# Performance work log

Hardware: AMD Instinct MI355X
Metric: run time of the kernel (lower is better)

## Reference

```python
import jax, jax.numpy as jnp
import numpy as np

MODES = 2
LC = 4
N = 6000
KNN = 10
NODES = 64
CH = MODES ** 2
M = N * 2 * (KNN + 1)  # total candidate couplings


def setup_inputs() -> dict:
    key = jax.random.key(0)
    ks = jax.random.split(key, 6)
    return {
        "CK_inputs": jax.random.normal(ks[0], (N, 2 * (KNN + 1), 3), dtype=jnp.float32),
        "W_in": jax.random.normal(ks[1], (3, NODES), dtype=jnp.float32) * 0.1,
        "b_in": jnp.zeros((NODES,), dtype=jnp.float32),
        "W_hid": jax.random.normal(ks[2], (LC - 1, NODES, NODES), dtype=jnp.float32) * 0.1,
        "b_hid": jnp.zeros((LC - 1, NODES), dtype=jnp.float32),
        "W_out": jax.random.normal(ks[3], (NODES, CH), dtype=jnp.float32) * 0.1,
        "b_out": jnp.zeros((CH,), dtype=jnp.float32),
        "coo": jax.random.randint(ks[4], (2, M), 0, N, dtype=jnp.int32),
    }


def _mlp(x, W_in, b_in, W_hid, b_hid, W_out, b_out):
    # MLP: 3 -> 64, (LC-1) hidden 64->64 layers, 64 -> CH; ReLU activations.
    h = jax.nn.relu(x @ W_in + b_in)
    for i in range(W_hid.shape[0]):  # small fixed layer count
        h = jax.nn.relu(h @ W_hid[i] + b_hid[i])
    return h @ W_out + b_out  # [M, CH]


def reference(CK_inputs, W_in, b_in, W_hid, b_hid, W_out, b_out, coo):
    C_stripped = _mlp(CK_inputs.reshape(-1, 3), W_in, b_in, W_hid, b_hid, W_out, b_out)  # [M, CH]
    D = MODES * N
    # Original: for channel ch = mi*MODES+mj, scatter C_stripped[:, ch] at indices coo*MODES+mj
    # (mj added to BOTH row and col, replicating the source exactly). Indices are
    # independent of mi, so sum over mi first, then one scatter-add per mj.
    vals = C_stripped.reshape(-1, MODES, MODES).sum(axis=1)  # [M, MODES]; axis1=mi, axis2=mj
    dense = jnp.zeros((D, D), dtype=CK_inputs.dtype)
    for mj in range(MODES):
        idx = coo * MODES + mj  # [2, M]
        dense = dense.at[idx[0], idx[1]].add(vals[:, mj])
    return dense
```

## Files before the change

kernel.cpp:

```cpp
#include <hip/hip_runtime.h>
#include <stdint.h>

#define NN    6000
#define KNNC  10
#define MM    (NN * 2 * (KNNC + 1))
#define DD    (2 * NN)
#define LCH   3
#define BLK   256

#define MLP_BLOCKS  ((MM + BLK - 1) / BLK)
#define FILL_BLOCKS 2048

__global__ __launch_bounds__(BLK) void fused_mlp_zero(
    const float* __restrict__ CK,
    const float* __restrict__ Win,
    const float* __restrict__ bin,
    const float* __restrict__ Whid,
    const float* __restrict__ bhid,
    const float* __restrict__ Wout,
    const float* __restrict__ bout,
    float* __restrict__ vals,
    float* __restrict__ out)
{
    const int tid = threadIdx.x;

    if (blockIdx.x >= MLP_BLOCKS) {
        const int fb = blockIdx.x - MLP_BLOCKS;
        float4 z = make_float4(0.f, 0.f, 0.f, 0.f);
        float4* outv = (float4*)out;
        const long long NV = (long long)DD * DD / 4;
        long long i = (long long)fb * BLK + tid;
        const long long stride = (long long)FILL_BLOCKS * BLK;
        for (; i < NV; i += stride) outv[i] = z;
        return;
    }

    const int m = blockIdx.x * BLK + tid;
    if (m >= MM) return;

    const float x0 = CK[m * 3 + 0];
    const float x1 = CK[m * 3 + 1];
    const float x2 = CK[m * 3 + 2];

    float h[64];
#pragma unroll
    for (int j = 0; j < 64; j++) {
        float a = bin[j];
        a = fmaf(x0, Win[j],       a);
        a = fmaf(x1, Win[64 + j],  a);
        a = fmaf(x2, Win[128 + j], a);
        h[j] = fmaxf(a, 0.0f);
    }

    for (int l = 0; l < LCH; l++) {
        const float* __restrict__ W  = Whid + (l << 12);
        const float* __restrict__ bh = bhid + (l << 6);
        float g[64];
#pragma unroll
        for (int j = 0; j < 64; j++) g[j] = bh[j];
        for (int k = 0; k < 64; k++) {
            const float hk = h[k];
            const float* __restrict__ Wk = W + (k << 6);
#pragma unroll
            for (int j = 0; j < 64; j++) g[j] = fmaf(Wk[j], hk, g[j]);
        }
#pragma unroll
        for (int j = 0; j < 64; j++) h[j] = fmaxf(g[j], 0.0f);
    }

    float v0 = bout[0] + bout[2];
    float v1 = bout[1] + bout[3];
#pragma unroll
    for (int k = 0; k < 64; k++) {
        v0 = fmaf(h[k], Wout[k * 4 + 0] + Wout[k * 4 + 2], v0);
        v1 = fmaf(h[k], Wout[k * 4 + 1] + Wout[k * 4 + 3], v1);
    }
    vals[m * 2 + 0] = v0;
    vals[m * 2 + 1] = v1;
}

__global__ __launch_bounds__(BLK) void scatter_add(
    const float* __restrict__ vals,
    const int* __restrict__ coo,
    float* __restrict__ out)
{
    const int t = blockIdx.x * BLK + threadIdx.x;
    if (t >= MM) return;
    const int r2 = coo[t] * 2;
    const int c2 = coo[MM + t] * 2;
    const float v0 = vals[t * 2 + 0];
    const float v1 = vals[t * 2 + 1];
    const long long f0 = (long long)r2 * DD + c2;
    atomicAdd(out + f0, v0);
    atomicAdd(out + f0 + DD + 1, v1);
}

extern "C" void kernel_launch(void* const* d_in, const int* in_sizes, int n_in,
                              void* d_out, int out_size, void* d_ws, size_t ws_size,
                              hipStream_t stream) {
    const float* CK   = (const float*)d_in[0];
    const float* Win  = (const float*)d_in[1];
    const float* bin  = (const float*)d_in[2];
    const float* Whid = (const float*)d_in[3];
    const float* bhid = (const float*)d_in[4];
    const float* Wout = (const float*)d_in[5];
    const float* bout = (const float*)d_in[6];
    const int* coo    = (const int*)d_in[7];
    float* out        = (float*)d_out;
    float* vals       = (float*)d_ws;

    fused_mlp_zero<<<MLP_BLOCKS + FILL_BLOCKS, BLK, 0, stream>>>(
        CK, Win, bin, Whid, bhid, Wout, bout, vals, out);
    scatter_add<<<MLP_BLOCKS, BLK, 0, stream>>>(vals, coo, out);
}
```

Baseline: 711.4 us.

## Interleave MLP and zero-fill waves within each block with nontemporal stores

Each 256-thread block now runs one MLP wave of 64 rows and three waves that zero-fill the 576 MB output, with the MLP wave's slot rotating across blocks. This is meant to overlap compute-bound MLP work with the bandwidth-bound fill on every CU, instead of running them in separate blocks. The fill uses nontemporal vector stores to avoid polluting cache, and the hidden-layer loops are kept rolled with unroll 1 to limit code size. In exchange, the MLP now gets only a quarter of the threads per block.

```diff
diff --git a/kernel.cpp b/kernel.cpp
--- a/kernel.cpp
+++ b/kernel.cpp
@@ -8,8 +8,10 @@
 #define LCH   3
 #define BLK   256
 
-#define MLP_BLOCKS  ((MM + BLK - 1) / BLK)
-#define FILL_BLOCKS 2048
+#define FBLOCKS ((MM + 63) / 64)
+#define NV      ((long long)DD * DD / 4)
+
+typedef float v4f __attribute__((ext_vector_type(4)));
 
 __global__ __launch_bounds__(BLK) void fused_mlp_zero(
     const float* __restrict__ CK,
@@ -22,20 +24,23 @@
     float* __restrict__ vals,
     float* __restrict__ out)
 {
-    const int tid = threadIdx.x;
+    const int tid  = threadIdx.x;
+    const int wave = tid >> 6;
+    const int lane = tid & 63;
+    const int mlpw = blockIdx.x & 3;
 
-    if (blockIdx.x >= MLP_BLOCKS) {
-        const int fb = blockIdx.x - MLP_BLOCKS;
-        float4 z = make_float4(0.f, 0.f, 0.f, 0.f);
-        float4* outv = (float4*)out;
-        const long long NV = (long long)DD * DD / 4;
-        long long i = (long long)fb * BLK + tid;
-        const long long stride = (long long)FILL_BLOCKS * BLK;
-        for (; i < NV; i += stride) outv[i] = z;
+    if (wave != mlpw) {
+        const int fw = wave - (wave > mlpw ? 1 : 0);
+        const long long ft = (long long)blockIdx.x * 192 + fw * 64 + lane;
+        const long long stride = (long long)FBLOCKS * 192;
+        v4f z = (v4f){0.f, 0.f, 0.f, 0.f};
+        v4f* outv = (v4f*)out;
+        for (long long i = ft; i < NV; i += stride)
+            __builtin_nontemporal_store(z, outv + i);
         return;
     }
 
-    const int m = blockIdx.x * BLK + tid;
+    const int m = blockIdx.x * 64 + lane;
     if (m >= MM) return;
 
     const float x0 = CK[m * 3 + 0];
@@ -52,12 +57,14 @@
         h[j] = fmaxf(a, 0.0f);
     }
 
+#pragma unroll 1
     for (int l = 0; l < LCH; l++) {
         const float* __restrict__ W  = Whid + (l << 12);
         const float* __restrict__ bh = bhid + (l << 6);
         float g[64];
 #pragma unroll
         for (int j = 0; j < 64; j++) g[j] = bh[j];
+#pragma unroll 1
         for (int k = 0; k < 64; k++) {
             const float hk = h[k];
             const float* __restrict__ Wk = W + (k << 6);
@@ -109,7 +116,7 @@
     float* out        = (float*)d_out;
     float* vals       = (float*)d_ws;
 
-    fused_mlp_zero<<<MLP_BLOCKS + FILL_BLOCKS, BLK, 0, stream>>>(
+    fused_mlp_zero<<<FBLOCKS, BLK, 0, stream>>>(
         CK, Win, bin, Whid, bhid, Wout, bout, vals, out);
-    scatter_add<<<MLP_BLOCKS, BLK, 0, stream>>>(vals, coo, out);
+    scatter_add<<<(MM + BLK - 1) / BLK, BLK, 0, stream>>>(vals, coo, out);
 }
```

New measurement: 734.2 us. 1.03x slower.

## Bucket MLP outputs by row and zero-fill plus scatter per row-pair block

Applied to the files above, without the earlier changes.

The MLP kernel now appends each coupling's (column, value pair) into a per-row bucket, using an atomic counter per row and a capped overflow list. A new per-row kernel zeroes its two output rows and applies that row's bucket entries with atomics into cache-resident lines, replacing the global zero fill and the random global scatter. A third kernel applies any overflow entries. The hidden-layer loop is also kept rolled. This adds counter atomics and a memset, and the fixed capacity caps mean results are wrong if the overflow exceeds MAX_OVF.

```diff
diff --git a/kernel.cpp b/kernel.cpp
--- a/kernel.cpp
+++ b/kernel.cpp
@@ -8,10 +8,15 @@
 #define LCH   3
 #define BLK   256
 
-#define MLP_BLOCKS  ((MM + BLK - 1) / BLK)
-#define FILL_BLOCKS 2048
+#define MLP_BLOCKS ((MM + BLK - 1) / BLK)
+#define CAP     96
+#define OVF_IDX 8064
+#define MAX_OVF 4096
 
-__global__ __launch_bounds__(BLK) void fused_mlp_zero(
+#define BUCKET_OFF  32768
+#define OVF_OFF     (BUCKET_OFF + 6000 * CAP * 16)
+
+__global__ __launch_bounds__(BLK) void mlp_bucket(
     const float* __restrict__ CK,
     const float* __restrict__ Win,
     const float* __restrict__ bin,
@@ -19,23 +24,12 @@
     const float* __restrict__ bhid,
     const float* __restrict__ Wout,
     const float* __restrict__ bout,
-    float* __restrict__ vals,
-    float* __restrict__ out)
+    const int*   __restrict__ coo,
+    int*    __restrict__ cnt,
+    float4* __restrict__ bucket,
+    int4*   __restrict__ ovf)
 {
-    const int tid = threadIdx.x;
-
-    if (blockIdx.x >= MLP_BLOCKS) {
-        const int fb = blockIdx.x - MLP_BLOCKS;
-        float4 z = make_float4(0.f, 0.f, 0.f, 0.f);
-        float4* outv = (float4*)out;
-        const long long NV = (long long)DD * DD / 4;
-        long long i = (long long)fb * BLK + tid;
-        const long long stride = (long long)FILL_BLOCKS * BLK;
-        for (; i < NV; i += stride) outv[i] = z;
-        return;
-    }
-
-    const int m = blockIdx.x * BLK + tid;
+    const int m = blockIdx.x * BLK + threadIdx.x;
     if (m >= MM) return;
 
     const float x0 = CK[m * 3 + 0];
@@ -52,6 +46,7 @@
         h[j] = fmaxf(a, 0.0f);
     }
 
+#pragma unroll 1
     for (int l = 0; l < LCH; l++) {
         const float* __restrict__ W  = Whid + (l << 12);
         const float* __restrict__ bh = bhid + (l << 6);
@@ -75,24 +70,52 @@
         v0 = fmaf(h[k], Wout[k * 4 + 0] + Wout[k * 4 + 2], v0);
         v1 = fmaf(h[k], Wout[k * 4 + 1] + Wout[k * 4 + 3], v1);
     }
-    vals[m * 2 + 0] = v0;
-    vals[m * 2 + 1] = v1;
+
+    const int r  = coo[m];
+    const int c2 = coo[MM + m] * 2;
+    const int slot = atomicAdd(&cnt[r], 1);
+    if (slot < CAP) {
+        bucket[r * CAP + slot] = make_float4(__int_as_float(c2), v0, v1, 0.f);
+    } else {
+        const int o = atomicAdd(&cnt[OVF_IDX], 1);
+        if (o < MAX_OVF)
+            ovf[o] = make_int4(r, c2, __float_as_int(v0), __float_as_int(v1));
+    }
 }
 
-__global__ __launch_bounds__(BLK) void scatter_add(
-    const float* __restrict__ vals,
-    const int* __restrict__ coo,
-    float* __restrict__ out)
+__global__ __launch_bounds__(BLK) void fill_patch(
+    const int*    __restrict__ cnt,
+    const float4* __restrict__ bucket,
+    float*        __restrict__ out)
 {
+    const int b = blockIdx.x;
+    float* rowbase = out + (long long)b * 2 * DD;
+    float4* dst = (float4*)rowbase;
+    const float4 z = make_float4(0.f, 0.f, 0.f, 0.f);
+    for (int i = threadIdx.x; i < 6000; i += BLK) dst[i] = z;
+    __syncthreads();
+
+    const int n = min(cnt[b], CAP);
+    for (int t = threadIdx.x; t < n; t += BLK) {
+        float4 e = bucket[b * CAP + t];
+        const int c2 = __float_as_int(e.x);
+        atomicAdd(rowbase + c2, e.y);
+        atomicAdd(rowbase + DD + c2 + 1, e.z);
+    }
+}
+
+__global__ __launch_bounds__(BLK) void ovf_apply(
+    const int*  __restrict__ cnt,
+    const int4* __restrict__ ovf,
+    float*      __restrict__ out)
+{
+    const int n = min(cnt[OVF_IDX], MAX_OVF);
     const int t = blockIdx.x * BLK + threadIdx.x;
-    if (t >= MM) return;
-    const int r2 = coo[t] * 2;
-    const int c2 = coo[MM + t] * 2;
-    const float v0 = vals[t * 2 + 0];
-    const float v1 = vals[t * 2 + 1];
-    const long long f0 = (long long)r2 * DD + c2;
-    atomicAdd(out + f0, v0);
-    atomicAdd(out + f0 + DD + 1, v1);
+    if (t >= n) return;
+    int4 e = ovf[t];
+    float* rowbase = out + (long long)e.x * 2 * DD;
+    atomicAdd(rowbase + e.y, __int_as_float(e.z));
+    atomicAdd(rowbase + DD + e.y + 1, __int_as_float(e.w));
 }
 
 extern "C" void kernel_launch(void* const* d_in, const int* in_sizes, int n_in,
@@ -107,9 +130,14 @@
     const float* bout = (const float*)d_in[6];
     const int* coo    = (const int*)d_in[7];
     float* out        = (float*)d_out;
-    float* vals       = (float*)d_ws;
 
-    fused_mlp_zero<<<MLP_BLOCKS + FILL_BLOCKS, BLK, 0, stream>>>(
-        CK, Win, bin, Whid, bhid, Wout, bout, vals, out);
-    scatter_add<<<MLP_BLOCKS, BLK, 0, stream>>>(vals, coo, out);
+    int*    cnt    = (int*)d_ws;
+    float4* bucket = (float4*)((char*)d_ws + BUCKET_OFF);
+    int4*   ovf    = (int4*)((char*)d_ws + OVF_OFF);
+
+    hipMemsetAsync(cnt, 0, 32768, stream);
+    mlp_bucket<<<MLP_BLOCKS, BLK, 0, stream>>>(
+        CK, Win, bin, Whid, bhid, Wout, bout, coo, cnt, bucket, ovf);
+    fill_patch<<<NN, BLK, 0, stream>>>(cnt, bucket, out);
+    ovf_apply<<<(MAX_OVF + BLK - 1) / BLK, BLK, 0, stream>>>(cnt, ovf, out);
 }
```

Result: no change. 722.9 us (+1.6%).
